# Kernel tuning notes

Hardware: AMD Instinct MI355X
Metric: run time of the kernel (lower is better)

## Reference

```python
import jax, jax.numpy as jnp
import numpy as np


def _conv1x1(x, w, b=None):
    # x: (N,C,H,W), w: (O,C) -> (N,O,H,W)
    y = jnp.einsum('nchw,oc->nohw', x, w)
    return y if b is None else y + b[None, :, None, None]


def _norm(f):
    # per-channel zero-mean / unit-std over (N,H,W); torch.std is unbiased (ddof=1)
    mean = f.mean(axis=(0, 2, 3), keepdims=True)
    std = f.std(axis=(0, 2, 3), ddof=1, keepdims=True)
    return (f - mean) / (std + 1e-6)


def _causal_attention(x, w_cls):
    N, C, H, W = x.shape
    M = _conv1x1(x, w_cls).reshape(N, -1, H * W)     # (N,K,HW)
    sm = jax.nn.softmax(M, axis=2)                   # softmax over spatial
    return jnp.einsum('nkp,ncp->nkc', sm, x.reshape(N, C, H * W))  # (N,K,C)


def _ccnet(x, wq, bq, wk, bk, wv, bv, gamma1):
    B, C, H, W = x.shape
    q = _conv1x1(x, wq, bq)  # (B,Cq,H,W)
    k = _conv1x1(x, wk, bk)
    v = _conv1x1(x, wv, bv)  # (B,C,H,W)
    # column (vertical) attention energies with -inf on the self diagonal
    eH = jnp.einsum('bciw,bcjw->biwj', q, k)         # (B,H,W,H)
    eH = jnp.where(jnp.eye(H, dtype=bool)[None, :, None, :], -jnp.inf, eH)
    # row (horizontal) attention energies
    eW = jnp.einsum('bchi,bchj->bhij', q, k)         # (B,H,W,W)
    att = jax.nn.softmax(jnp.concatenate([eH, eW], axis=3), axis=3)
    attH, attW = att[..., :H], att[..., H:]
    outH = jnp.einsum('bcjw,biwj->bciw', v, attH)    # aggregate along column
    outW = jnp.einsum('bchj,bhij->bchi', v, attW)    # aggregate along row
    return gamma1 * (outH + outW) + x


def setup_inputs() -> dict:
    key = jax.random.key(0)
    ks = jax.random.split(key, 10)
    B, C, H, W = 8, 256, 96, 96
    Cq, K = C // 8, 6
    f32 = jnp.float32
    return {
        'preds_S': jax.random.normal(ks[0], (B, C, H, W), f32),
        'preds_T': jax.random.normal(ks[1], (B, C, H, W), f32),
        'w_cls': jax.random.normal(ks[2], (K, C), f32) * 0.05,
        'wq': jax.random.normal(ks[3], (Cq, C), f32) * 0.05,
        'bq': jnp.zeros((Cq,), f32),
        'wk': jax.random.normal(ks[4], (Cq, C), f32) * 0.05,
        'bk': jnp.zeros((Cq,), f32),
        'wv': jax.random.normal(ks[5], (C, C), f32) * 0.05,
        'bv': jnp.zeros((C,), f32),
        'gamma1': jax.random.normal(ks[6], (1,), f32) * 0.1,
    }


def reference(preds_S, preds_T, w_cls, wq, bq, wk, bk, wv, bv, gamma1):
    CA_W, CC_W = 0.0005, 1e-05
    N = preds_S.shape[0]
    s = _norm(preds_S)
    t = _norm(preds_T)
    ca_t = _causal_attention(t, w_cls)
    ca_s = _causal_attention(s, w_cls)
    ca_loss = jnp.sum((ca_t - ca_s) ** 2) / N
    cc_t = _ccnet(t, wq, bq, wk, bk, wv, bv, gamma1)
    cc_s = _ccnet(s, wq, bq, wk, bk, wv, bv, gamma1)
    cc_loss = jnp.sum((cc_t - cc_s) ** 2) / N
    return ca_loss * CA_W + cc_loss * CC_W
```

## Files before the change

### kernel.cpp

```cpp
#include <hip/hip_runtime.h>
#include <math.h>

#define NBAT 8
#define NC   256
#define NH   96
#define NW   96
#define NP   9216
#define NCQ  32
#define NKC  6
#define NL   192
#define NV   320
#define NTOT 73728

typedef __attribute__((ext_vector_type(4))) float  floatx4;
typedef __attribute__((ext_vector_type(8))) short  short8;

__device__ __forceinline__ float bf2f(unsigned short h){
  return __uint_as_float(((unsigned)h) << 16);
}
__device__ __forceinline__ float bflo(unsigned u){ return __uint_as_float(u << 16); }
__device__ __forceinline__ float bfhi(unsigned u){ return __uint_as_float(u & 0xFFFF0000u); }
__device__ __forceinline__ unsigned short f2bf(float f){
  unsigned u = __float_as_uint(f);
  u += 0x7FFFu + ((u >> 16) & 1u);
  return (unsigned short)(u >> 16);
}

union F4 { float4 v; float a[4]; };

__device__ __forceinline__ float warpReduceSum(float v){
  #pragma unroll
  for (int m = 32; m; m >>= 1) v += __shfl_xor(v, m);
  return v;
}
__device__ __forceinline__ float warpReduceMax(float v){
  #pragma unroll
  for (int m = 32; m; m >>= 1) v = fmaxf(v, __shfl_xor(v, m));
  return v;
}
__device__ float blockReduceSum(float v){
  __shared__ float lds[8];
  v = warpReduceSum(v);
  int wid = threadIdx.x >> 6, lane = threadIdx.x & 63;
  int nw = blockDim.x >> 6;
  if (lane == 0) lds[wid] = v;
  __syncthreads();
  if (wid == 0){
    v = (lane < nw) ? lds[lane] : 0.f;
    #pragma unroll
    for (int m = 4; m; m >>= 1) v += __shfl_xor(v, m);
  }
  __syncthreads();
  return v;
}
__device__ float blockReduceMax(float v){
  __shared__ float lds[8];
  v = warpReduceMax(v);
  int wid = threadIdx.x >> 6, lane = threadIdx.x & 63;
  int nw = blockDim.x >> 6;
  if (lane == 0) lds[wid] = v;
  __syncthreads();
  if (wid == 0){
    v = (lane < nw) ? lds[lane] : -INFINITY;
    #pragma unroll
    for (int m = 4; m; m >>= 1) v = fmaxf(v, __shfl_xor(v, m));
  }
  __syncthreads();
  return v;
}

__global__ __launch_bounds__(256)
void k_stats(const float* __restrict__ S, const float* __restrict__ T,
             float* __restrict__ s_sum, float* __restrict__ s_sq){
  int blk = blockIdx.x;
  int t = blk / (NC * NBAT);
  int rem = blk % (NC * NBAT);
  int c = rem / NBAT;
  int n = rem % NBAT;
  const float4* x4 = (const float4*)((t ? T : S) + ((size_t)n * NC + c) * NP);
  float s = 0.f, q = 0.f;
  for (int p = threadIdx.x; p < NP / 4; p += 256){
    F4 f; f.v = x4[p];
    #pragma unroll
    for (int j = 0; j < 4; j++){ s += f.a[j]; q += f.a[j] * f.a[j]; }
  }
  s = blockReduceSum(s);
  q = blockReduceSum(q);
  if (threadIdx.x == 0){
    atomicAdd(&s_sum[t * NC + c], s);
    atomicAdd(&s_sq[t * NC + c], q);
  }
}

__global__ __launch_bounds__(512)
void k_finalize(const float* __restrict__ s_sum, const float* __restrict__ s_sq,
                float* __restrict__ mean, float* __restrict__ inv){
  int i = threadIdx.x;
  if (i < 2 * NC){
    float s = s_sum[i], q = s_sq[i];
    float m = s / (float)NTOT;
    float var = (q - s * m) / (float)(NTOT - 1);
    var = fmaxf(var, 0.f);
    mean[i] = m;
    inv[i] = 1.f / (sqrtf(var) + 1e-6f);
  }
}

__global__ __launch_bounds__(256)
void k_xn(const float* __restrict__ x0, int b0,
          const float* __restrict__ mean, const float* __restrict__ inv, int t,
          unsigned short* __restrict__ XN){
  int pt = blockIdx.x, ct = blockIdx.y, bb = blockIdx.z;
  int bg = b0 + bb;
  int p0 = pt * 64, c0 = ct * 64;
  __shared__ float tile[64 * 65];
  const float* x = x0 + ((size_t)bg * NC + c0) * NP + p0;
  #pragma unroll
  for (int i = 0; i < 4; i++){
    int idx = threadIdx.x + i * 256;
    int r = idx >> 4, g = (idx & 15) * 4;
    F4 f; f.v = *(const float4*)(x + (size_t)r * NP + g);
    float m = mean[t * NC + c0 + r], iv = inv[t * NC + c0 + r];
    #pragma unroll
    for (int j = 0; j < 4; j++) tile[(g + j) * 65 + r] = (f.a[j] - m) * iv;
  }
  __syncthreads();
  #pragma unroll
  for (int i = 0; i < 4; i++){
    int idx = threadIdx.x + i * 256;
    int p = idx >> 4, g = (idx & 15) * 4;
    unsigned lo = (unsigned)f2bf(tile[p * 65 + g + 0]) | ((unsigned)f2bf(tile[p * 65 + g + 1]) << 16);
    unsigned hi = (unsigned)f2bf(tile[p * 65 + g + 2]) | ((unsigned)f2bf(tile[p * 65 + g + 3]) << 16);
    uint2 u; u.x = lo; u.y = hi;
    *(uint2*)(XN + ((size_t)bb * NP + p0 + p) * NC + c0 + g) = u;
  }
}

__global__ __launch_bounds__(256)
void k_wconv(const float* __restrict__ wv, const float* __restrict__ wq,
             const float* __restrict__ wk, unsigned short* __restrict__ Wb){
  int n = blockIdx.x;
  const float* src = (n < 256) ? (wv + (size_t)n * NC)
                   : (n < 288) ? (wq + (size_t)(n - 256) * NC)
                               : (wk + (size_t)(n - 288) * NC);
  Wb[(size_t)n * NC + threadIdx.x] = f2bf(src[threadIdx.x]);
}

__global__ __launch_bounds__(256)
void k_caMB(const unsigned short* __restrict__ XN, const float* __restrict__ wcls,
            float* __restrict__ smca){
  int pt = blockIdx.x, bb = blockIdx.y;
  __shared__ float wl[NKC * NC];
  for (int idx = threadIdx.x; idx < NKC * NC; idx += 256) wl[idx] = wcls[idx];
  __syncthreads();
  int p = pt * 256 + threadIdx.x;
  const unsigned short* xr = XN + ((size_t)bb * NP + p) * NC;
  float acc[NKC] = {};
  for (int g = 0; g < 32; g++){
    short8 x8 = *(const short8*)(xr + g * 8);
    #pragma unroll
    for (int e = 0; e < 8; e++){
      float xv = bf2f(((unsigned short*)&x8)[e]);
      int c = g * 8 + e;
      #pragma unroll
      for (int k = 0; k < NKC; k++) acc[k] += wl[k * NC + c] * xv;
    }
  }
  #pragma unroll
  for (int k = 0; k < NKC; k++) smca[((size_t)bb * NKC + k) * NP + p] = acc[k];
}

__global__ __launch_bounds__(256)
void k_caSoftmax(float* __restrict__ smca){
  int r = blockIdx.x;
  float* row = smca + (size_t)r * NP;
  float m = -INFINITY;
  for (int p = threadIdx.x; p < NP; p += 256) m = fmaxf(m, row[p]);
  m = blockReduceMax(m);
  __shared__ float bm, bs;
  if (threadIdx.x == 0) bm = m;
  __syncthreads();
  m = bm;
  float s = 0.f;
  for (int p = threadIdx.x; p < NP; p += 256) s += expf(row[p] - m);
  s = blockReduceSum(s);
  if (threadIdx.x == 0) bs = 1.f / s;
  __syncthreads();
  float rs = bs;
  for (int p = threadIdx.x; p < NP; p += 256) row[p] = expf(row[p] - m) * rs;
}

__global__ __launch_bounds__(256)
void k_caOutB(const unsigned short* __restrict__ XN, const float* __restrict__ smca,
              float* __restrict__ ca, int t, int b0){
  int ks = blockIdx.x, bb = blockIdx.y;
  __shared__ float sml[NKC * 1152];
  __shared__ float lca[NKC * NC];
  int p0 = ks * 1152;
  const float* smb = smca + (size_t)bb * NKC * NP;
  for (int idx = threadIdx.x; idx < NKC * 1152; idx += 256){
    int k = idx / 1152, pp = idx % 1152;
    sml[idx] = smb[(size_t)k * NP + p0 + pp];
  }
  for (int idx = threadIdx.x; idx < NKC * NC; idx += 256) lca[idx] = 0.f;
  __syncthreads();
  int c8 = (threadIdx.x & 31) * 8, psub = threadIdx.x >> 5;
  const unsigned short* xb = XN + (size_t)bb * NP * NC;
  float acc[NKC][8] = {};
  for (int j = 0; j < 144; j++){
    int pp = psub + 8 * j;
    short8 x8 = *(const short8*)(xb + (size_t)(p0 + pp) * NC + c8);
    float xf[8];
    #pragma unroll
    for (int e = 0; e < 8; e++) xf[e] = bf2f(((unsigned short*)&x8)[e]);
    #pragma unroll
    for (int k = 0; k < NKC; k++){
      float sv = sml[k * 1152 + pp];
      #pragma unroll
      for (int e = 0; e < 8; e++) acc[k][e] += sv * xf[e];
    }
  }
  #pragma unroll
  for (int k = 0; k < NKC; k++)
    #pragma unroll
    for (int e = 0; e < 8; e++) atomicAdd(&lca[k * NC + c8 + e], acc[k][e]);
  __syncthreads();
  int n = b0 + bb;
  #pragma unroll
  for (int k = 0; k < NKC; k++)
    atomicAdd(&ca[((size_t)(t * NBAT + n) * NKC + k) * NC + threadIdx.x],
              lca[k * NC + threadIdx.x]);
}

__global__ __launch_bounds__(256)
void k_caLoss(const float* __restrict__ ca, float* __restrict__ out){
  int i = blockIdx.x * 256 + threadIdx.x;
  float d = 0.f;
  if (i < NBAT * NKC * NC) d = ca[(size_t)NBAT * NKC * NC + i] - ca[i];
  float ss = blockReduceSum(d * d);
  if (threadIdx.x == 0) atomicAdd(out, ss * (0.0005f / 8.0f));
}

__global__ __launch_bounds__(256)
void k_v(const unsigned short* __restrict__ XN, const unsigned short* __restrict__ Wb,
         const float* __restrict__ bv, const float* __restrict__ bq,
         const float* __restrict__ bk,
         unsigned short* __restrict__ VT1,
         unsigned short* __restrict__ qb, unsigned short* __restrict__ kb){
  int pt = blockIdx.x, bb = blockIdx.y;
  int p0 = pt * 64;
  __shared__ unsigned short Wl[NV * 40];
  int lane = threadIdx.x & 63;
  int wid = threadIdx.x >> 6;
  int col = lane & 15, quad = lane >> 4;
  const unsigned short* xnb = XN + (size_t)bb * NP * NC + (size_t)(p0 + wid * 16 + col) * NC;
  floatx4 acc[20];
  #pragma unroll
  for (int nt = 0; nt < 20; nt++) acc[nt] = (floatx4){0.f, 0.f, 0.f, 0.f};

  int ci_n[5], ci_k8[5];
  #pragma unroll
  for (int i = 0; i < 5; i++){ int ci = i * 256 + threadIdx.x; ci_n[i] = ci >> 2; ci_k8[i] = (ci & 3) * 8; }

  short8 w[5];
  #pragma unroll
  for (int i = 0; i < 5; i++)
    w[i] = *(const short8*)(Wb + (size_t)ci_n[i] * NC + ci_k8[i]);

  for (int ks = 0; ks < 8; ks++){
    if (ks) __syncthreads();
    #pragma unroll
    for (int i = 0; i < 5; i++)
      *(short8*)(Wl + ci_n[i] * 40 + ci_k8[i]) = w[i];
    __syncthreads();
    if (ks < 7){
      int k0n = (ks + 1) * 32;
      #pragma unroll
      for (int i = 0; i < 5; i++)
        w[i] = *(const short8*)(Wb + (size_t)ci_n[i] * NC + k0n + ci_k8[i]);
    }
    short8 a = *(const short8*)(xnb + ks * 32 + quad * 8);
    #pragma unroll
    for (int nt = 0; nt < 20; nt++){
      short8 b = *(const short8*)(Wl + (nt * 16 + col) * 40 + quad * 8);
      acc[nt] = __builtin_amdgcn_mfma_f32_16x16x32_bf16(a, b, acc[nt], 0, 0, 0);
    }
  }

  int prow0 = p0 + wid * 16 + quad * 4;
  #pragma unroll
  for (int nt = 0; nt < 16; nt++){
    int c = nt * 16 + col;
    float bias = bv[c];
    uint2 u;
    u.x = (unsigned)f2bf(acc[nt][0] + bias) | ((unsigned)f2bf(acc[nt][1] + bias) << 16);
    u.y = (unsigned)f2bf(acc[nt][2] + bias) | ((unsigned)f2bf(acc[nt][3] + bias) << 16);
    *(uint2*)(VT1 + ((size_t)bb * NC + c) * NP + prow0) = u;
  }
  #pragma unroll
  for (int nt = 16; nt < 18; nt++){
    int c = (nt - 16) * 16 + col;
    float bias = bq[c];
    #pragma unroll
    for (int i = 0; i < 4; i++)
      qb[((size_t)bb * NP + prow0 + i) * NCQ + c] = f2bf(acc[nt][i] + bias);
  }
  #pragma unroll
  for (int nt = 18; nt < 20; nt++){
    int c = (nt - 18) * 16 + col;
    float bias = bk[c];
    #pragma unroll
    for (int i = 0; i < 4; i++)
      kb[((size_t)bb * NP + prow0 + i) * NCQ + c] = f2bf(acc[nt][i] + bias);
  }
}

__global__ __launch_bounds__(256)
void k_vt(const unsigned short* __restrict__ VT1, unsigned short* __restrict__ VT2){
  int c = blockIdx.x, bb = blockIdx.y;
  __shared__ unsigned short tile[96 * 104];
  size_t base = ((size_t)bb * NC + c) * NP;
  for (int idx = threadIdx.x; idx < 1152; idx += 256){
    int h = idx / 12, g = idx % 12;
    short8 v = *(const short8*)(VT1 + base + h * 96 + g * 8);
    #pragma unroll
    for (int kk = 0; kk < 8; kk++) tile[(g * 8 + kk) * 104 + h] = ((unsigned short*)&v)[kk];
  }
  __syncthreads();
  for (int idx = threadIdx.x; idx < 1152; idx += 256){
    int w = idx / 12, g = idx % 12;
    short8 v = *(const short8*)(tile + w * 104 + g * 8);
    *(short8*)(VT2 + base + w * 96 + g * 8) = v;
  }
}

__global__ __launch_bounds__(256)
void k_eH(const unsigned short* __restrict__ qb, const unsigned short* __restrict__ kb,
          unsigned short* __restrict__ att){
  int w = blockIdx.x, bb = blockIdx.y;
  int lane = threadIdx.x & 63, wid = threadIdx.x >> 6;
  int col = lane & 15, quad = lane >> 4;
  int mi0 = (wid & 1) * 3, ni0 = (wid >> 1) * 3;
  short8 a[3], b[3];
  #pragma unroll
  for (int m = 0; m < 3; m++)
    a[m] = *(const short8*)(qb + ((size_t)bb * NP + ((mi0 + m) * 16 + col) * 96 + w) * NCQ + quad * 8);
  #pragma unroll
  for (int n = 0; n < 3; n++)
    b[n] = *(const short8*)(kb + ((size_t)bb * NP + ((ni0 + n) * 16 + col) * 96 + w) * NCQ + quad * 8);
  floatx4 acc[3][3];
  #pragma unroll
  for (int m = 0; m < 3; m++)
    #pragma unroll
    for (int n = 0; n < 3; n++){
      acc[m][n] = (floatx4){0.f, 0.f, 0.f, 0.f};
      acc[m][n] = __builtin_amdgcn_mfma_f32_16x16x32_bf16(a[m], b[n], acc[m][n], 0, 0, 0);
    }
  #pragma unroll
  for (int m = 0; m < 3; m++)
    #pragma unroll
    for (int n = 0; n < 3; n++){
      int j = (ni0 + n) * 16 + col;
      #pragma unroll
      for (int r = 0; r < 4; r++){
        int i = (mi0 + m) * 16 + quad * 4 + r;
        float v = (j == i) ? -INFINITY : acc[m][n][r];
        att[((size_t)bb * NP + i * 96 + w) * NL + j] = f2bf(v);
      }
    }
}

__global__ __launch_bounds__(256)
void k_eW(const unsigned short* __restrict__ qb, const unsigned short* __restrict__ kb,
          unsigned short* __restrict__ att){
  int h = blockIdx.x, bb = blockIdx.y;
  int lane = threadIdx.x & 63, wid = threadIdx.x >> 6;
  int col = lane & 15, quad = lane >> 4;
  int mi0 = (wid & 1) * 3, ni0 = (wid >> 1) * 3;
  short8 a[3], b[3];
  #pragma unroll
  for (int m = 0; m < 3; m++)
    a[m] = *(const short8*)(qb + ((size_t)bb * NP + h * 96 + (mi0 + m) * 16 + col) * NCQ + quad * 8);
  #pragma unroll
  for (int n = 0; n < 3; n++)
    b[n] = *(const short8*)(kb + ((size_t)bb * NP + h * 96 + (ni0 + n) * 16 + col) * NCQ + quad * 8);
  floatx4 acc[3][3];
  #pragma unroll
  for (int m = 0; m < 3; m++)
    #pragma unroll
    for (int n = 0; n < 3; n++){
      acc[m][n] = (floatx4){0.f, 0.f, 0.f, 0.f};
      acc[m][n] = __builtin_amdgcn_mfma_f32_16x16x32_bf16(a[m], b[n], acc[m][n], 0, 0, 0);
    }
  #pragma unroll
  for (int m = 0; m < 3; m++)
    #pragma unroll
    for (int n = 0; n < 3; n++){
      int j = (ni0 + n) * 16 + col;
      #pragma unroll
      for (int r = 0; r < 4; r++){
        int i = (mi0 + m) * 16 + quad * 4 + r;
        att[((size_t)bb * NP + h * 96 + i) * NL + 96 + j] = f2bf(acc[m][n][r]);
      }
    }
}

__global__ __launch_bounds__(256)
void k_attSoftmax(unsigned short* __restrict__ att){
  int q = blockIdx.x * 4 + (threadIdx.x >> 6);
  int lane = threadIdx.x & 63;
  unsigned short* row = att + (size_t)q * NL;
  float e0 = bf2f(row[lane]);
  float e1 = bf2f(row[64 + lane]);
  float e2 = bf2f(row[128 + lane]);
  float m = fmaxf(e0, fmaxf(e1, e2));
  m = warpReduceMax(m);
  float x0 = expf(e0 - m), x1 = expf(e1 - m), x2 = expf(e2 - m);
  float s = warpReduceSum(x0 + x1 + x2);
  float rs = 1.f / s;
  row[lane]       = f2bf(x0 * rs);
  row[64 + lane]  = f2bf(x1 * rs);
  row[128 + lane] = f2bf(x2 * rs);
}

__global__ __launch_bounds__(256)
void k_outH(const unsigned short* __restrict__ VT2, const unsigned short* __restrict__ att,
            unsigned short* __restrict__ OH){
  int w = blockIdx.x, bb = blockIdx.y;
  int lane = threadIdx.x & 63, wid = threadIdx.x >> 6;
  int col = lane & 15, quad = lane >> 4;
  floatx4 acc[4][6];
  #pragma unroll
  for (int ct = 0; ct < 4; ct++)
    #pragma unroll
    for (int it = 0; it < 6; it++) acc[ct][it] = (floatx4){0.f, 0.f, 0.f, 0.f};
  #pragma unroll
  for (int ks = 0; ks < 3; ks++){
    int k0 = ks * 32 + quad * 8;
    short8 a[4], b[6];
    #pragma unroll
    for (int ct = 0; ct < 4; ct++){
      int c = wid * 64 + ct * 16 + col;
      a[ct] = *(const short8*)(VT2 + ((size_t)bb * NC + c) * NP + w * 96 + k0);
    }
    #pragma unroll
    for (int it = 0; it < 6; it++){
      int i = it * 16 + col;
      b[it] = *(const short8*)(att + ((size_t)bb * NP + i * 96 + w) * NL + k0);
    }
    #pragma unroll
    for (int ct = 0; ct < 4; ct++)
      #pragma unroll
      for (int it = 0; it < 6; it++)
        acc[ct][it] = __builtin_amdgcn_mfma_f32_16x16x32_bf16(a[ct], b[it], acc[ct][it], 0, 0, 0);
  }
  #pragma unroll
  for (int ct = 0; ct < 4; ct++)
    #pragma unroll
    for (int it = 0; it < 6; it++){
      int c0 = wid * 64 + ct * 16 + quad * 4;
      int i = it * 16 + col;
      uint2 u;
      u.x = (unsigned)f2bf(acc[ct][it][0]) | ((unsigned)f2bf(acc[ct][it][1]) << 16);
      u.y = (unsigned)f2bf(acc[ct][it][2]) | ((unsigned)f2bf(acc[ct][it][3]) << 16);
      *(uint2*)(OH + ((size_t)bb * NP + i * 96 + w) * NC + c0) = u;
    }
}

__global__ __launch_bounds__(256)
void k_outW(const unsigned short* __restrict__ VT1, const unsigned short* __restrict__ att,
            const unsigned short* __restrict__ OH, unsigned short* __restrict__ OtL,
            const unsigned short* __restrict__ XN,
            const float* __restrict__ gamma, int spass,
            float* __restrict__ out){
  int h = blockIdx.x, bb = blockIdx.y;
  int lane = threadIdx.x & 63, wid = threadIdx.x >> 6;
  int col = lane & 15, quad = lane >> 4;
  float g = gamma[0];
  floatx4 acc[4][6];
  #pragma unroll
  for (int ct = 0; ct < 4; ct++)
    #pragma unroll
    for (int it = 0; it < 6; it++) acc[ct][it] = (floatx4){0.f, 0.f, 0.f, 0.f};
  #pragma unroll
  for (int ks = 0; ks < 3; ks++){
    int k0 = ks * 32 + quad * 8;
    short8 a[4], b[6];
    #pragma unroll
    for (int ct = 0; ct < 4; ct++){
      int c = wid * 64 + ct * 16 + col;
      a[ct] = *(const short8*)(VT1 + ((size_t)bb * NC + c) * NP + h * 96 + k0);
    }
    #pragma unroll
    for (int it = 0; it < 6; it++){
      int i = it * 16 + col;
      b[it] = *(const short8*)(att + ((size_t)bb * NP + h * 96 + i) * NL + 96 + k0);
    }
    #pragma unroll
    for (int ct = 0; ct < 4; ct++)
      #pragma unroll
      for (int it = 0; it < 6; it++)
        acc[ct][it] = __builtin_amdgcn_mfma_f32_16x16x32_bf16(a[ct], b[it], acc[ct][it], 0, 0, 0);
  }
  if (!spass){
    #pragma unroll
    for (int ct = 0; ct < 4; ct++)
      #pragma unroll
      for (int it = 0; it < 6; it++){
        int c0 = wid * 64 + ct * 16 + quad * 4;
        int i = it * 16 + col;
        size_t base = ((size_t)bb * NP + h * 96 + i) * NC + c0;
        uint2 uoh = *(const uint2*)(OH + base);
        uint2 uxn = *(const uint2*)(XN + base);
        float o0 = g * (acc[ct][it][0] + bflo(uoh.x)) + bflo(uxn.x);
        float o1 = g * (acc[ct][it][1] + bfhi(uoh.x)) + bfhi(uxn.x);
        float o2 = g * (acc[ct][it][2] + bflo(uoh.y)) + bflo(uxn.y);
        float o3 = g * (acc[ct][it][3] + bfhi(uoh.y)) + bfhi(uxn.y);
        uint2 u;
        u.x = (unsigned)f2bf(o0) | ((unsigned)f2bf(o1) << 16);
        u.y = (unsigned)f2bf(o2) | ((unsigned)f2bf(o3) << 16);
        *(uint2*)(OtL + base) = u;
      }
  } else {
    float ss = 0.f;
    #pragma unroll
    for (int ct = 0; ct < 4; ct++)
      #pragma unroll
      for (int it = 0; it < 6; it++){
        int c0 = wid * 64 + ct * 16 + quad * 4;
        int i = it * 16 + col;
        size_t base = ((size_t)bb * NP + h * 96 + i) * NC + c0;
        uint2 uoh = *(const uint2*)(OH + base);
        uint2 uxn = *(const uint2*)(XN + base);
        uint2 uot = *(const uint2*)(OtL + base);
        float d0 = bflo(uot.x) - (g * (acc[ct][it][0] + bflo(uoh.x)) + bflo(uxn.x));
        float d1 = bfhi(uot.x) - (g * (acc[ct][it][1] + bfhi(uoh.x)) + bfhi(uxn.x));
        float d2 = bflo(uot.y) - (g * (acc[ct][it][2] + bflo(uoh.y)) + bflo(uxn.y));
        float d3 = bfhi(uot.y) - (g * (acc[ct][it][3] + bfhi(uoh.y)) + bfhi(uxn.y));
        ss += d0 * d0 + d1 * d1 + d2 * d2 + d3 * d3;
      }
    ss = blockReduceSum(ss);
    if (threadIdx.x == 0) atomicAdd(out, ss * (1e-5f / 8.0f));
  }
}

extern "C" void kernel_launch(void* const* d_in, const int* in_sizes, int n_in,
                              void* d_out, int out_size, void* d_ws, size_t ws_size,
                              hipStream_t stream){
  (void)in_sizes; (void)n_in; (void)out_size;
  const float* S    = (const float*)d_in[0];
  const float* T    = (const float*)d_in[1];
  const float* wcls = (const float*)d_in[2];
  const float* wq   = (const float*)d_in[3];
  const float* bq   = (const float*)d_in[4];
  const float* wk   = (const float*)d_in[5];
  const float* bk   = (const float*)d_in[6];
  const float* wv   = (const float*)d_in[7];
  const float* bv   = (const float*)d_in[8];
  const float* gamma= (const float*)d_in[9];
  float* out = (float*)d_out;

  char* base = (char*)d_ws;
  size_t off = 0;
  auto alloc = [&](size_t b){ size_t o = off; off += (b + 255) & ~(size_t)255; return o; };
  size_t o_ssum = alloc(2 * NC * 4);
  size_t o_ssq  = alloc(2 * NC * 4);
  size_t o_mean = alloc(2 * NC * 4);
  size_t o_inv  = alloc(2 * NC * 4);
  size_t o_wb   = alloc((size_t)NV * NC * 2);
  size_t o_ca   = alloc((size_t)2 * NBAT * NKC * NC * 4);
  size_t fixed = off;
  size_t per_b = (size_t)NP * NC * 2 * 5
               + (size_t)NP * NCQ * 2 * 2
               + (size_t)NP * NL * 2
               + (size_t)NKC * NP * 4;
  int NB = 8;
  while (NB > 1 && fixed + (size_t)NB * per_b + 8192 > ws_size) NB >>= 1;

  size_t o_xn  = alloc((size_t)NB * NP * NC * 2);
  size_t o_v1  = alloc((size_t)NB * NP * NC * 2);
  size_t o_v2  = alloc((size_t)NB * NP * NC * 2);
  size_t o_q   = alloc((size_t)NB * NP * NCQ * 2);
  size_t o_k   = alloc((size_t)NB * NP * NCQ * 2);
  size_t o_att = alloc((size_t)NB * NP * NL * 2);
  size_t o_oh  = alloc((size_t)NB * NP * NC * 2);
  size_t o_ot  = alloc((size_t)NB * NP * NC * 2);
  size_t o_sm  = alloc((size_t)NB * NKC * NP * 4);

  float* ssum = (float*)(base + o_ssum);
  float* ssq  = (float*)(base + o_ssq);
  float* mean = (float*)(base + o_mean);
  float* inv  = (float*)(base + o_inv);
  float* ca   = (float*)(base + o_ca);
  float* smca = (float*)(base + o_sm);
  unsigned short* Wb  = (unsigned short*)(base + o_wb);
  unsigned short* XN  = (unsigned short*)(base + o_xn);
  unsigned short* VT1 = (unsigned short*)(base + o_v1);
  unsigned short* VT2 = (unsigned short*)(base + o_v2);
  unsigned short* qbp = (unsigned short*)(base + o_q);
  unsigned short* kbp = (unsigned short*)(base + o_k);
  unsigned short* att = (unsigned short*)(base + o_att);
  unsigned short* OH  = (unsigned short*)(base + o_oh);
  unsigned short* OtL = (unsigned short*)(base + o_ot);

  hipMemsetAsync(d_out, 0, 4, stream);
  hipMemsetAsync(base + o_ssum, 0, 4096, stream);
  hipMemsetAsync(base + o_ca, 0, (size_t)2 * NBAT * NKC * NC * 4, stream);

  k_stats<<<dim3(2 * NC * NBAT), 256, 0, stream>>>(S, T, ssum, ssq);
  k_finalize<<<1, 512, 0, stream>>>(ssum, ssq, mean, inv);
  k_wconv<<<dim3(NV), 256, 0, stream>>>(wv, wq, wk, Wb);

  for (int b0 = 0; b0 < NBAT; b0 += NB){
    for (int pass = 0; pass < 2; pass++){
      int t = (pass == 0) ? 1 : 0;
      const float* x = t ? T : S;
      k_xn<<<dim3(144, 4, NB), 256, 0, stream>>>(x, b0, mean, inv, t, XN);
      k_caMB<<<dim3(36, NB), 256, 0, stream>>>(XN, wcls, smca);
      k_caSoftmax<<<dim3(NB * NKC), 256, 0, stream>>>(smca);
      k_caOutB<<<dim3(8, NB), 256, 0, stream>>>(XN, smca, ca, t, b0);
      k_v<<<dim3(144, NB), 256, 0, stream>>>(XN, Wb, bv, bq, bk, VT1, qbp, kbp);
      k_vt<<<dim3(NC, NB), 256, 0, stream>>>(VT1, VT2);
      k_eH<<<dim3(96, NB), 256, 0, stream>>>(qbp, kbp, att);
      k_eW<<<dim3(96, NB), 256, 0, stream>>>(qbp, kbp, att);
      k_attSoftmax<<<dim3(NB * 2304), 256, 0, stream>>>(att);
      k_outH<<<dim3(96, NB), 256, 0, stream>>>(VT2, att, OH);
      k_outW<<<dim3(96, NB), 256, 0, stream>>>(VT1, att, OH, OtL, XN,
                                               gamma, pass, out);
    }
  }
  k_caLoss<<<dim3(48), 256, 0, stream>>>(ca, out);
}
```

Measured before the change: 696.9 us.

## Fuse causal-attention softmax into logits kernel and merge energy kernels

The separate spatial softmax kernel is removed. The logits kernel now writes exp(logit) and atomically accumulates per-row sums, and the output kernel applies 1/sum when it accumulates. The output kernel also splits channels into two halves to double the grid, and reduces across lanes with shuffles before the LDS atomics. The eH and eW energy kernels are merged into one launch over a z dimension. Dropping max subtraction risks exp overflow for large logits, which is safe only because the normalized inputs and small weights keep logits small.

```diff
diff --git a/kernel.cpp b/kernel.cpp
--- a/kernel.cpp
+++ b/kernel.cpp
@@ -33,11 +33,6 @@
   for (int m = 32; m; m >>= 1) v += __shfl_xor(v, m);
   return v;
 }
-__device__ __forceinline__ float warpReduceMax(float v){
-  #pragma unroll
-  for (int m = 32; m; m >>= 1) v = fmaxf(v, __shfl_xor(v, m));
-  return v;
-}
 __device__ float blockReduceSum(float v){
   __shared__ float lds[8];
   v = warpReduceSum(v);
@@ -49,21 +44,6 @@
     v = (lane < nw) ? lds[lane] : 0.f;
     #pragma unroll
     for (int m = 4; m; m >>= 1) v += __shfl_xor(v, m);
-  }
-  __syncthreads();
-  return v;
-}
-__device__ float blockReduceMax(float v){
-  __shared__ float lds[8];
-  v = warpReduceMax(v);
-  int wid = threadIdx.x >> 6, lane = threadIdx.x & 63;
-  int nw = blockDim.x >> 6;
-  if (lane == 0) lds[wid] = v;
-  __syncthreads();
-  if (wid == 0){
-    v = (lane < nw) ? lds[lane] : -INFINITY;
-    #pragma unroll
-    for (int m = 4; m; m >>= 1) v = fmaxf(v, __shfl_xor(v, m));
   }
   __syncthreads();
   return v;
@@ -148,7 +128,7 @@
 
 __global__ __launch_bounds__(256)
 void k_caMB(const unsigned short* __restrict__ XN, const float* __restrict__ wcls,
-            float* __restrict__ smca){
+            float* __restrict__ smca, float* __restrict__ casum, int t, int b0){
   int pt = blockIdx.x, bb = blockIdx.y;
   __shared__ float wl[NKC * NC];
   for (int idx = threadIdx.x; idx < NKC * NC; idx += 256) wl[idx] = wcls[idx];
@@ -166,49 +146,37 @@
       for (int k = 0; k < NKC; k++) acc[k] += wl[k * NC + c] * xv;
     }
   }
-  #pragma unroll
-  for (int k = 0; k < NKC; k++) smca[((size_t)bb * NKC + k) * NP + p] = acc[k];
-}
-
-__global__ __launch_bounds__(256)
-void k_caSoftmax(float* __restrict__ smca){
-  int r = blockIdx.x;
-  float* row = smca + (size_t)r * NP;
-  float m = -INFINITY;
-  for (int p = threadIdx.x; p < NP; p += 256) m = fmaxf(m, row[p]);
-  m = blockReduceMax(m);
-  __shared__ float bm, bs;
-  if (threadIdx.x == 0) bm = m;
-  __syncthreads();
-  m = bm;
-  float s = 0.f;
-  for (int p = threadIdx.x; p < NP; p += 256) s += expf(row[p] - m);
-  s = blockReduceSum(s);
-  if (threadIdx.x == 0) bs = 1.f / s;
-  __syncthreads();
-  float rs = bs;
-  for (int p = threadIdx.x; p < NP; p += 256) row[p] = expf(row[p] - m) * rs;
+  int lane = threadIdx.x & 63;
+  int n = b0 + bb;
+  #pragma unroll
+  for (int k = 0; k < NKC; k++){
+    float ev = expf(acc[k]);
+    smca[((size_t)bb * NKC + k) * NP + p] = ev;
+    float ws = warpReduceSum(ev);
+    if (lane == 0) atomicAdd(&casum[(t * NBAT + n) * NKC + k], ws);
+  }
 }
 
 __global__ __launch_bounds__(256)
 void k_caOutB(const unsigned short* __restrict__ XN, const float* __restrict__ smca,
-              float* __restrict__ ca, int t, int b0){
-  int ks = blockIdx.x, bb = blockIdx.y;
+              const float* __restrict__ casum, float* __restrict__ ca, int t, int b0){
+  int ks = blockIdx.x, cs = blockIdx.y, bb = blockIdx.z;
   __shared__ float sml[NKC * 1152];
-  __shared__ float lca[NKC * NC];
-  int p0 = ks * 1152;
+  __shared__ float lca[NKC * 128];
+  int p0 = ks * 1152, cbase = cs * 128;
   const float* smb = smca + (size_t)bb * NKC * NP;
   for (int idx = threadIdx.x; idx < NKC * 1152; idx += 256){
     int k = idx / 1152, pp = idx % 1152;
     sml[idx] = smb[(size_t)k * NP + p0 + pp];
   }
-  for (int idx = threadIdx.x; idx < NKC * NC; idx += 256) lca[idx] = 0.f;
-  __syncthreads();
-  int c8 = (threadIdx.x & 31) * 8, psub = threadIdx.x >> 5;
+  for (int idx = threadIdx.x; idx < NKC * 128; idx += 256) lca[idx] = 0.f;
+  __syncthreads();
+  int c8 = cbase + (threadIdx.x & 15) * 8;
+  int psub = threadIdx.x >> 4;
   const unsigned short* xb = XN + (size_t)bb * NP * NC;
   float acc[NKC][8] = {};
-  for (int j = 0; j < 144; j++){
-    int pp = psub + 8 * j;
+  for (int j = 0; j < 72; j++){
+    int pp = psub + 16 * j;
     short8 x8 = *(const short8*)(xb + (size_t)(p0 + pp) * NC + c8);
     float xf[8];
     #pragma unroll
@@ -223,13 +191,27 @@
   #pragma unroll
   for (int k = 0; k < NKC; k++)
     #pragma unroll
-    for (int e = 0; e < 8; e++) atomicAdd(&lca[k * NC + c8 + e], acc[k][e]);
+    for (int e = 0; e < 8; e++){
+      float v = acc[k][e];
+      v += __shfl_xor(v, 16);
+      v += __shfl_xor(v, 32);
+      acc[k][e] = v;
+    }
+  if ((threadIdx.x & 48) == 0){
+    #pragma unroll
+    for (int k = 0; k < NKC; k++)
+      #pragma unroll
+      for (int e = 0; e < 8; e++)
+        atomicAdd(&lca[k * 128 + (c8 - cbase) + e], acc[k][e]);
+  }
   __syncthreads();
   int n = b0 + bb;
-  #pragma unroll
-  for (int k = 0; k < NKC; k++)
-    atomicAdd(&ca[((size_t)(t * NBAT + n) * NKC + k) * NC + threadIdx.x],
-              lca[k * NC + threadIdx.x]);
+  for (int idx = threadIdx.x; idx < NKC * 128; idx += 256){
+    int k = idx >> 7, cc = idx & 127;
+    float scale = 1.f / casum[(t * NBAT + n) * NKC + k];
+    atomicAdd(&ca[((size_t)(t * NBAT + n) * NKC + k) * NC + cbase + cc],
+              lca[idx] * scale);
+  }
 }
 
 __global__ __launch_bounds__(256)
@@ -335,19 +317,25 @@
 }
 
 __global__ __launch_bounds__(256)
-void k_eH(const unsigned short* __restrict__ qb, const unsigned short* __restrict__ kb,
-          unsigned short* __restrict__ att){
-  int w = blockIdx.x, bb = blockIdx.y;
+void k_e(const unsigned short* __restrict__ qb, const unsigned short* __restrict__ kb,
+         unsigned short* __restrict__ att){
+  int x = blockIdx.x, bb = blockIdx.y, which = blockIdx.z;
   int lane = threadIdx.x & 63, wid = threadIdx.x >> 6;
   int col = lane & 15, quad = lane >> 4;
   int mi0 = (wid & 1) * 3, ni0 = (wid >> 1) * 3;
   short8 a[3], b[3];
   #pragma unroll
-  for (int m = 0; m < 3; m++)
-    a[m] = *(const short8*)(qb + ((size_t)bb * NP + ((mi0 + m) * 16 + col) * 96 + w) * NCQ + quad * 8);
-  #pragma unroll
-  for (int n = 0; n < 3; n++)
-    b[n] = *(const short8*)(kb + ((size_t)bb * NP + ((ni0 + n) * 16 + col) * 96 + w) * NCQ + quad * 8);
+  for (int m = 0; m < 3; m++){
+    int r = (mi0 + m) * 16 + col;
+    size_t pa = which ? ((size_t)x * 96 + r) : ((size_t)r * 96 + x);
+    a[m] = *(const short8*)(qb + ((size_t)bb * NP + pa) * NCQ + quad * 8);
+  }
+  #pragma unroll
+  for (int n = 0; n < 3; n++){
+    int r = (ni0 + n) * 16 + col;
+    size_t pa = which ? ((size_t)x * 96 + r) : ((size_t)r * 96 + x);
+    b[n] = *(const short8*)(kb + ((size_t)bb * NP + pa) * NCQ + quad * 8);
+  }
   floatx4 acc[3][3];
   #pragma unroll
   for (int m = 0; m < 3; m++)
@@ -364,43 +352,10 @@
       #pragma unroll
       for (int r = 0; r < 4; r++){
         int i = (mi0 + m) * 16 + quad * 4 + r;
-        float v = (j == i) ? -INFINITY : acc[m][n][r];
-        att[((size_t)bb * NP + i * 96 + w) * NL + j] = f2bf(v);
-      }
-    }
-}
-
-__global__ __launch_bounds__(256)
-void k_eW(const unsigned short* __restrict__ qb, const unsigned short* __restrict__ kb,
-          unsigned short* __restrict__ att){
-  int h = blockIdx.x, bb = blockIdx.y;
-  int lane = threadIdx.x & 63, wid = threadIdx.x >> 6;
-  int col = lane & 15, quad = lane >> 4;
-  int mi0 = (wid & 1) * 3, ni0 = (wid >> 1) * 3;
-  short8 a[3], b[3];
-  #pragma unroll
-  for (int m = 0; m < 3; m++)
-    a[m] = *(const short8*)(qb + ((size_t)bb * NP + h * 96 + (mi0 + m) * 16 + col) * NCQ + quad * 8);
-  #pragma unroll
-  for (int n = 0; n < 3; n++)
-    b[n] = *(const short8*)(kb + ((size_t)bb * NP + h * 96 + (ni0 + n) * 16 + col) * NCQ + quad * 8);
-  floatx4 acc[3][3];
-  #pragma unroll
-  for (int m = 0; m < 3; m++)
-    #pragma unroll
-    for (int n = 0; n < 3; n++){
-      acc[m][n] = (floatx4){0.f, 0.f, 0.f, 0.f};
-      acc[m][n] = __builtin_amdgcn_mfma_f32_16x16x32_bf16(a[m], b[n], acc[m][n], 0, 0, 0);
-    }
-  #pragma unroll
-  for (int m = 0; m < 3; m++)
-    #pragma unroll
-    for (int n = 0; n < 3; n++){
-      int j = (ni0 + n) * 16 + col;
-      #pragma unroll
-      for (int r = 0; r < 4; r++){
-        int i = (mi0 + m) * 16 + quad * 4 + r;
-        att[((size_t)bb * NP + h * 96 + i) * NL + 96 + j] = f2bf(acc[m][n][r]);
+        float v = acc[m][n][r];
+        if (!which && j == i) v = -INFINITY;
+        size_t row = which ? ((size_t)x * 96 + i) : ((size_t)i * 96 + x);
+        att[((size_t)bb * NP + row) * NL + (which ? 96 + j : j)] = f2bf(v);
       }
     }
 }
@@ -414,7 +369,8 @@
   float e1 = bf2f(row[64 + lane]);
   float e2 = bf2f(row[128 + lane]);
   float m = fmaxf(e0, fmaxf(e1, e2));
-  m = warpReduceMax(m);
+  #pragma unroll
+  for (int s = 32; s; s >>= 1) m = fmaxf(m, __shfl_xor(m, s));
   float x0 = expf(e0 - m), x1 = expf(e1 - m), x2 = expf(e2 - m);
   float s = warpReduceSum(x0 + x1 + x2);
   float rs = 1.f / s;
@@ -569,6 +525,7 @@
   size_t o_inv  = alloc(2 * NC * 4);
   size_t o_wb   = alloc((size_t)NV * NC * 2);
   size_t o_ca   = alloc((size_t)2 * NBAT * NKC * NC * 4);
+  size_t o_csum = alloc((size_t)2 * NBAT * NKC * 4);
   size_t fixed = off;
   size_t per_b = (size_t)NP * NC * 2 * 5
                + (size_t)NP * NCQ * 2 * 2
@@ -592,6 +549,7 @@
   float* mean = (float*)(base + o_mean);
   float* inv  = (float*)(base + o_inv);
   float* ca   = (float*)(base + o_ca);
+  float* csum = (float*)(base + o_csum);
   float* smca = (float*)(base + o_sm);
   unsigned short* Wb  = (unsigned short*)(base + o_wb);
   unsigned short* XN  = (unsigned short*)(base + o_xn);
@@ -605,7 +563,9 @@
 
   hipMemsetAsync(d_out, 0, 4, stream);
   hipMemsetAsync(base + o_ssum, 0, 4096, stream);
-  hipMemsetAsync(base + o_ca, 0, (size_t)2 * NBAT * NKC * NC * 4, stream);
+  hipMemsetAsync(base + o_ca, 0,
+                 (size_t)2 * NBAT * NKC * NC * 4 + 256 + (size_t)2 * NBAT * NKC * 4,
+                 stream);
 
   k_stats<<<dim3(2 * NC * NBAT), 256, 0, stream>>>(S, T, ssum, ssq);
   k_finalize<<<1, 512, 0, stream>>>(ssum, ssq, mean, inv);
@@ -616,13 +576,11 @@
       int t = (pass == 0) ? 1 : 0;
       const float* x = t ? T : S;
       k_xn<<<dim3(144, 4, NB), 256, 0, stream>>>(x, b0, mean, inv, t, XN);
-      k_caMB<<<dim3(36, NB), 256, 0, stream>>>(XN, wcls, smca);
-      k_caSoftmax<<<dim3(NB * NKC), 256, 0, stream>>>(smca);
-      k_caOutB<<<dim3(8, NB), 256, 0, stream>>>(XN, smca, ca, t, b0);
+      k_caMB<<<dim3(36, NB), 256, 0, stream>>>(XN, wcls, smca, csum, t, b0);
+      k_caOutB<<<dim3(8, 2, NB), 256, 0, stream>>>(XN, smca, csum, ca, t, b0);
       k_v<<<dim3(144, NB), 256, 0, stream>>>(XN, Wb, bv, bq, bk, VT1, qbp, kbp);
       k_vt<<<dim3(NC, NB), 256, 0, stream>>>(VT1, VT2);
-      k_eH<<<dim3(96, NB), 256, 0, stream>>>(qbp, kbp, att);
-      k_eW<<<dim3(96, NB), 256, 0, stream>>>(qbp, kbp, att);
+      k_e<<<dim3(96, NB, 2), 256, 0, stream>>>(qbp, kbp, att);
       k_attSoftmax<<<dim3(NB * 2304), 256, 0, stream>>>(att);
       k_outH<<<dim3(96, NB), 256, 0, stream>>>(VT2, att, OH);
       k_outW<<<dim3(96, NB), 256, 0, stream>>>(VT1, att, OH, OtL, XN,
```

New measurement: 697.3 us. About the same (+0.1%).
